# Kernel tuning notes

Measured on AMD Instinct MI355X. Metric: run time of the kernel, lower is better.

Reference implementation:

```python
import jax, jax.numpy as jnp
import numpy as np

B, N, HD = 128, 8192, 256


def setup_inputs() -> dict:
    key = jax.random.key(0)
    ks = jax.random.split(key, 12)
    s = 1.0 / np.sqrt(HD)
    return {
        "encoder_outputs": jax.random.normal(ks[0], (B, N, HD), jnp.float32),
        "hidden": jax.random.normal(ks[1], (B, HD), jnp.float32),
        "cell": jax.random.normal(ks[2], (B, HD), jnp.float32),
        "end_node_embed": jax.random.normal(ks[3], (1, HD), jnp.float32),
        "initial_input": jax.random.normal(ks[4], (B, 3 * HD), jnp.float32),
        # LSTMCell params (PyTorch layout: gates ordered i, f, g, o)
        "W_ih": jax.random.uniform(ks[5], (4 * HD, 3 * HD), jnp.float32, -s, s),
        "b_ih": jax.random.uniform(ks[6], (4 * HD,), jnp.float32, -s, s),
        "W_hh": jax.random.uniform(ks[7], (4 * HD, HD), jnp.float32, -s, s),
        "b_hh": jax.random.uniform(ks[8], (4 * HD,), jnp.float32, -s, s),
        # query_transform Linear params
        "Wq": jax.random.uniform(ks[9], (HD, HD), jnp.float32, -s, s),
        "bq": jax.random.uniform(ks[10], (HD,), jnp.float32, -s, s),
        "max_steps": 10,
    }


def reference(encoder_outputs, hidden, cell, end_node_embed, initial_input,
              W_ih, b_ih, W_hh, b_hh, Wq, bq, max_steps):
    # Prediction mode (teacher_indices=None): feed back top-3 gathered embeddings.
    def step(carry, _):
        h, c, x = carry
        gates = x @ W_ih.T + b_ih + h @ W_hh.T + b_hh        # (B, 4*HD)
        i, f, g, o = jnp.split(gates, 4, axis=-1)
        c_new = jax.nn.sigmoid(f) * c + jax.nn.sigmoid(i) * jnp.tanh(g)
        h_new = jax.nn.sigmoid(o) * jnp.tanh(c_new)
        query = h_new @ Wq.T + bq                            # (B, HD)
        logits = jnp.einsum('bd,bnd->bn', query, encoder_outputs)  # (B, N)
        _, top3 = jax.lax.top_k(logits, 3)                   # (B, 3) int32
        vecs = jnp.take_along_axis(encoder_outputs, top3[..., None], axis=1)  # (B, 3, HD)
        x_next = vecs.reshape(x.shape[0], -1)                # (B, 3*HD)
        return (h_new, c_new, x_next), (logits, top3)
    _, (logits_all, idx_all) = jax.lax.scan(
        step, (hidden, cell, initial_input), None, length=max_steps)
    return logits_all, idx_all  # (max_steps, B, N), (max_steps, B, 3)
```

## Files before the change

### kernel.cpp

```cpp
#include <hip/hip_runtime.h>

typedef unsigned short u16;
typedef unsigned int   u32;

#define B_    128
#define N_    8192
#define HD_   256
#define X_    768
#define T_    10
#define SEGS_ 16
#define SEGROWS_ 512

__device__ float g_h[B_*HD_];
__device__ float g_c[B_*HD_];
__device__ float g_q[B_*HD_];
__device__ float g_pval[B_*SEGS_*3];
__device__ int   g_pidx[B_*SEGS_*3];
__device__ int   g_isf32;

__device__ __forceinline__ float bf2f(u16 u){ return __uint_as_float(((u32)u)<<16); }
__device__ __forceinline__ float lo2f(u32 w){ return __uint_as_float(w<<16); }
__device__ __forceinline__ float hi2f(u32 w){ return __uint_as_float(w & 0xffff0000u); }
__device__ __forceinline__ u16 f2bf(float f){
  u32 u = __float_as_uint(f);
  u32 r = u + 0x7fffu + ((u>>16)&1u);
  return (u16)(r>>16);
}

template<bool F32>
__device__ __forceinline__ float ld1(const void* p, size_t i){
  if constexpr (F32) return ((const float*)p)[i];
  else               return bf2f(((const u16*)p)[i]);
}

template<bool F32>
__device__ __forceinline__ void st1(void* p, size_t i, float v){
  if constexpr (F32) ((float*)p)[i] = v;
  else               ((u16*)p)[i]   = f2bf(v);
}

template<bool F32>
__device__ __forceinline__ void ld8(const void* p, size_t i, float* o){
  if constexpr (F32){
    const float4* q = (const float4*)((const float*)p + i);
    float4 a = q[0], b = q[1];
    o[0]=a.x; o[1]=a.y; o[2]=a.z; o[3]=a.w;
    o[4]=b.x; o[5]=b.y; o[6]=b.z; o[7]=b.w;
  } else {
    uint4 u = *(const uint4*)((const u16*)p + i);
    o[0]=lo2f(u.x); o[1]=hi2f(u.x); o[2]=lo2f(u.y); o[3]=hi2f(u.y);
    o[4]=lo2f(u.z); o[5]=hi2f(u.z); o[6]=lo2f(u.w); o[7]=hi2f(u.w);
  }
}

__device__ __forceinline__ void t3ins(float v,int i,
    float&v0,int&i0,float&v1,int&i1,float&v2,int&i2){
  if (v>v0 || (v==v0 && i<i0)) { v2=v1;i2=i1; v1=v0;i1=i0; v0=v;i0=i; }
  else if (v>v1 || (v==v1 && i<i1)) { v2=v1;i2=i1; v1=v;i1=i; }
  else if (v>v2 || (v==v2 && i<i2)) { v2=v;i2=i; }
}

__global__ void k_probe(const void* enc){
  const int lane = threadIdx.x;
  const u16 u = ((const u16*)enc)[lane*2];
  const float a = fabsf(bf2f(u));
  const bool inr = (a >= 0.0009765625f) && (a <= 1024.0f);
  unsigned long long m = __ballot(inr ? 1 : 0);
  if (lane==0) g_isf32 = (__popcll(m) < 32) ? 1 : 0;
}

template<bool F32>
__device__ void lstm_body(const void* enc, const void* h0, const void* c0,
  const void* x0, const void* Wih, const void* bih, const void* Whh,
  const void* bhh, const void* Wq, const void* bq, void* out, int t)
{
  const int b = blockIdx.x, d = threadIdx.x;
  __shared__ float xs[X_];
  __shared__ float hs[HD_];
  __shared__ float hn[HD_];
  __shared__ int   idx3[3];

  float cd;
  if (t == 0){
    for (int i=d;i<X_;i+=256) xs[i] = ld1<F32>(x0, (size_t)b*X_+i);
    hs[d] = ld1<F32>(h0, (size_t)b*HD_+d);
    cd    = ld1<F32>(c0, (size_t)b*HD_+d);
  } else {
    if (d==0){
      float v0=-3.4e38f,v1=-3.4e38f,v2=-3.4e38f; int i0=-1,i1=-1,i2=-1;
      const float* pv = g_pval + b*SEGS_*3;
      const int*   pi = g_pidx + b*SEGS_*3;
      for (int s=0;s<SEGS_*3;s++) t3ins(pv[s],pi[s],v0,i0,v1,i1,v2,i2);
      idx3[0]=i0; idx3[1]=i1; idx3[2]=i2;
      const size_t ib = (size_t)T_*B_*N_ + (size_t)(t-1)*B_*3 + (size_t)b*3;
      st1<F32>(out, ib+0, (float)i0);
      st1<F32>(out, ib+1, (float)i1);
      st1<F32>(out, ib+2, (float)i2);
    }
    __syncthreads();
    #pragma unroll
    for (int j=0;j<3;j++){
      int jj = idx3[j]; jj = jj<0 ? 0 : (jj>N_-1 ? N_-1 : jj);
      xs[j*HD_+d] = ld1<F32>(enc, ((size_t)b*N_ + jj)*HD_ + d);
    }
    hs[d] = g_h[b*HD_+d];
    cd    = g_c[b*HD_+d];
  }
  __syncthreads();

  float g4[4];
  #pragma unroll
  for (int gi=0;gi<4;gi++){
    const int row = gi*HD_ + d;
    float acc = ld1<F32>(bih,row) + ld1<F32>(bhh,row);
    #pragma unroll 4
    for (int kk=0;kk<X_/8;kk++){
      float w[8]; ld8<F32>(Wih, (size_t)row*X_ + kk*8, w);
      #pragma unroll
      for (int j=0;j<8;j++) acc = fmaf(xs[kk*8+j], w[j], acc);
    }
    #pragma unroll 4
    for (int kk=0;kk<HD_/8;kk++){
      float w[8]; ld8<F32>(Whh, (size_t)row*HD_ + kk*8, w);
      #pragma unroll
      for (int j=0;j<8;j++) acc = fmaf(hs[kk*8+j], w[j], acc);
    }
    g4[gi]=acc;
  }
  const float sig_i = 1.f/(1.f+expf(-g4[0]));
  const float sig_f = 1.f/(1.f+expf(-g4[1]));
  const float tan_g = tanhf(g4[2]);
  const float sig_o = 1.f/(1.f+expf(-g4[3]));
  const float cn = sig_f*cd + sig_i*tan_g;
  const float hv = sig_o*tanhf(cn);
  g_c[b*HD_+d]=cn; g_h[b*HD_+d]=hv; hn[d]=hv;
  __syncthreads();

  float acc = ld1<F32>(bq,d);
  #pragma unroll 4
  for (int kk=0;kk<HD_/8;kk++){
    float w[8]; ld8<F32>(Wq, (size_t)d*HD_ + kk*8, w);
    #pragma unroll
    for (int j=0;j<8;j++) acc = fmaf(hn[kk*8+j], w[j], acc);
  }
  g_q[b*HD_+d]=acc;
}

__global__ __launch_bounds__(256) void k_lstm(
  const void* enc, const void* h0, const void* c0, const void* x0,
  const void* Wih, const void* bih, const void* Whh, const void* bhh,
  const void* Wq, const void* bq, void* out, int t)
{
  if (g_isf32) lstm_body<true >(enc,h0,c0,x0,Wih,bih,Whh,bhh,Wq,bq,out,t);
  else         lstm_body<false>(enc,h0,c0,x0,Wih,bih,Whh,bhh,Wq,bq,out,t);
}

template<bool F32>
__device__ void logits_body(const void* enc, void* out, int t)
{
  const int seg = blockIdx.x, b = blockIdx.y;
  const int tid  = threadIdx.x;
  const int wave = tid>>6;
  const int lane = tid&63;
  const int kl   = lane&31;
  const int half = lane>>5;

  float qv[8];
  const float* qb = g_q + b*HD_ + kl*8;
  #pragma unroll
  for (int j=0;j<8;j++) qv[j]=qb[j];

  float v0=-3.4e38f,v1=-3.4e38f,v2=-3.4e38f; int i0=-1,i1=-1,i2=-1;
  const size_t rowbase = (size_t)b*N_ + seg*SEGROWS_;
  const size_t obase   = (size_t)t*B_*N_ + rowbase;

  #pragma unroll 2
  for (int it=0; it<SEGROWS_/8; ++it){
    const int n = (it*4 + wave)*2 + half;
    float w[8]; ld8<F32>(enc, (rowbase + n)*HD_ + kl*8, w);
    float acc =       qv[0]*w[0];
    acc = fmaf(qv[1], w[1], acc);
    acc = fmaf(qv[2], w[2], acc);
    acc = fmaf(qv[3], w[3], acc);
    acc = fmaf(qv[4], w[4], acc);
    acc = fmaf(qv[5], w[5], acc);
    acc = fmaf(qv[6], w[6], acc);
    acc = fmaf(qv[7], w[7], acc);
    #pragma unroll
    for (int off=16; off>=1; off>>=1)
      acc += __shfl_xor(acc, off, 64);
    if (kl==0) st1<F32>(out, obase + n, acc);
    t3ins(acc, seg*SEGROWS_+n, v0,i0,v1,i1,v2,i2);
  }

  __shared__ float sv[8][3];
  __shared__ int   si[8][3];
  if (kl==0){
    const int slot = wave*2+half;
    sv[slot][0]=v0; sv[slot][1]=v1; sv[slot][2]=v2;
    si[slot][0]=i0; si[slot][1]=i1; si[slot][2]=i2;
  }
  __syncthreads();
  if (tid==0){
    float w0=-3.4e38f,w1=-3.4e38f,w2=-3.4e38f; int j0=-1,j1=-1,j2=-1;
    for (int s=0;s<8;s++)
      for (int k=0;k<3;k++)
        t3ins(sv[s][k],si[s][k],w0,j0,w1,j1,w2,j2);
    float* pv = g_pval + (b*SEGS_+seg)*3;
    int*   pi = g_pidx + (b*SEGS_+seg)*3;
    pv[0]=w0; pv[1]=w1; pv[2]=w2;
    pi[0]=j0; pi[1]=j1; pi[2]=j2;
  }
}

__global__ __launch_bounds__(256) void k_logits(const void* enc, void* out, int t)
{
  if (g_isf32) logits_body<true >(enc,out,t);
  else         logits_body<false>(enc,out,t);
}

__global__ void k_final(void* out)
{
  const int b = blockIdx.x;
  if (threadIdx.x==0){
    float v0=-3.4e38f,v1=-3.4e38f,v2=-3.4e38f; int i0=-1,i1=-1,i2=-1;
    const float* pv = g_pval + b*SEGS_*3;
    const int*   pi = g_pidx + b*SEGS_*3;
    for (int s=0;s<SEGS_*3;s++) t3ins(pv[s],pi[s],v0,i0,v1,i1,v2,i2);
    const size_t ib = (size_t)T_*B_*N_ + (size_t)(T_-1)*B_*3 + (size_t)b*3;
    if (g_isf32){
      ((float*)out)[ib+0]=(float)i0;
      ((float*)out)[ib+1]=(float)i1;
      ((float*)out)[ib+2]=(float)i2;
    } else {
      ((u16*)out)[ib+0]=f2bf((float)i0);
      ((u16*)out)[ib+1]=f2bf((float)i1);
      ((u16*)out)[ib+2]=f2bf((float)i2);
    }
  }
}

extern "C" void kernel_launch(void* const* d_in, const int* in_sizes, int n_in,
                              void* d_out, int out_size, void* d_ws, size_t ws_size,
                              hipStream_t stream)
{
  (void)in_sizes; (void)n_in; (void)out_size; (void)d_ws; (void)ws_size;
  const void* enc = d_in[0];
  const void* h0  = d_in[1];
  const void* c0  = d_in[2];
  const void* x0  = d_in[4];
  const void* Wih = d_in[5];
  const void* bih = d_in[6];
  const void* Whh = d_in[7];
  const void* bhh = d_in[8];
  const void* Wq  = d_in[9];
  const void* bq  = d_in[10];

  k_probe<<<dim3(1),dim3(64),0,stream>>>(enc);

  for (int t=0;t<T_;t++){
    k_lstm<<<dim3(B_),dim3(256),0,stream>>>(enc,h0,c0,x0,Wih,bih,Whh,bhh,Wq,bq,
                                            d_out, t);
    k_logits<<<dim3(SEGS_,B_),dim3(256),0,stream>>>(enc, d_out, t);
  }
  k_final<<<dim3(B_),dim3(64),0,stream>>>(d_out);
}
```

Before: 4.655 ms.

## Fuse all timesteps into one persistent cooperative kernel with grid syncs

Replaces the 21 per-step kernel launches with a single cooperative persistent kernel. Blocks loop over the LSTM and logits work for each timestep and separate the phases with grid.sync(). The logits work is also regrouped into fewer, larger segments: 8 segments of 1024 rows instead of 16 of 512. This is meant to remove launch and drain gaps between the small LSTM kernel and the large logits kernel. In exchange it adds grid-wide barrier cost, and the LSTM phase only uses 128 blocks, leaving the rest idle at each step. If the cooperative launch is unavailable, the code falls back to the multi-kernel path.

```diff
diff --git a/kernel.cpp b/kernel.cpp
--- a/kernel.cpp
+++ b/kernel.cpp
@@ -1,4 +1,7 @@
 #include <hip/hip_runtime.h>
+#include <hip/hip_cooperative_groups.h>
+
+namespace cg = cooperative_groups;
 
 typedef unsigned short u16;
 typedef unsigned int   u32;
@@ -8,8 +11,9 @@
 #define HD_   256
 #define X_    768
 #define T_    10
-#define SEGS_ 16
-#define SEGROWS_ 512
+#define SEGS_ 8
+#define SEGROWS_ 1024
+#define PAIRS_ (B_*SEGS_)
 
 __device__ float g_h[B_*HD_];
 __device__ float g_c[B_*HD_];
@@ -17,6 +21,11 @@
 __device__ float g_pval[B_*SEGS_*3];
 __device__ int   g_pidx[B_*SEGS_*3];
 __device__ int   g_isf32;
+
+struct P {
+  const void *enc, *h0, *c0, *x0, *Wih, *bih, *Whh, *bhh, *Wq, *bq;
+  void* out;
+};
 
 __device__ __forceinline__ float bf2f(u16 u){ return __uint_as_float(((u32)u)<<16); }
 __device__ __forceinline__ float lo2f(u32 w){ return __uint_as_float(w<<16); }
@@ -70,11 +79,9 @@
 }
 
 template<bool F32>
-__device__ void lstm_body(const void* enc, const void* h0, const void* c0,
-  const void* x0, const void* Wih, const void* bih, const void* Whh,
-  const void* bhh, const void* Wq, const void* bq, void* out, int t)
-{
-  const int b = blockIdx.x, d = threadIdx.x;
+__device__ void lstm_b(const P& p, int t, int b)
+{
+  const int d = threadIdx.x;
   __shared__ float xs[X_];
   __shared__ float hs[HD_];
   __shared__ float hn[HD_];
@@ -82,9 +89,9 @@
 
   float cd;
   if (t == 0){
-    for (int i=d;i<X_;i+=256) xs[i] = ld1<F32>(x0, (size_t)b*X_+i);
-    hs[d] = ld1<F32>(h0, (size_t)b*HD_+d);
-    cd    = ld1<F32>(c0, (size_t)b*HD_+d);
+    for (int i=d;i<X_;i+=256) xs[i] = ld1<F32>(p.x0, (size_t)b*X_+i);
+    hs[d] = ld1<F32>(p.h0, (size_t)b*HD_+d);
+    cd    = ld1<F32>(p.c0, (size_t)b*HD_+d);
   } else {
     if (d==0){
       float v0=-3.4e38f,v1=-3.4e38f,v2=-3.4e38f; int i0=-1,i1=-1,i2=-1;
@@ -93,15 +100,15 @@
       for (int s=0;s<SEGS_*3;s++) t3ins(pv[s],pi[s],v0,i0,v1,i1,v2,i2);
       idx3[0]=i0; idx3[1]=i1; idx3[2]=i2;
       const size_t ib = (size_t)T_*B_*N_ + (size_t)(t-1)*B_*3 + (size_t)b*3;
-      st1<F32>(out, ib+0, (float)i0);
-      st1<F32>(out, ib+1, (float)i1);
-      st1<F32>(out, ib+2, (float)i2);
+      st1<F32>(p.out, ib+0, (float)i0);
+      st1<F32>(p.out, ib+1, (float)i1);
+      st1<F32>(p.out, ib+2, (float)i2);
     }
     __syncthreads();
     #pragma unroll
     for (int j=0;j<3;j++){
       int jj = idx3[j]; jj = jj<0 ? 0 : (jj>N_-1 ? N_-1 : jj);
-      xs[j*HD_+d] = ld1<F32>(enc, ((size_t)b*N_ + jj)*HD_ + d);
+      xs[j*HD_+d] = ld1<F32>(p.enc, ((size_t)b*N_ + jj)*HD_ + d);
     }
     hs[d] = g_h[b*HD_+d];
     cd    = g_c[b*HD_+d];
@@ -112,16 +119,16 @@
   #pragma unroll
   for (int gi=0;gi<4;gi++){
     const int row = gi*HD_ + d;
-    float acc = ld1<F32>(bih,row) + ld1<F32>(bhh,row);
+    float acc = ld1<F32>(p.bih,row) + ld1<F32>(p.bhh,row);
     #pragma unroll 4
     for (int kk=0;kk<X_/8;kk++){
-      float w[8]; ld8<F32>(Wih, (size_t)row*X_ + kk*8, w);
+      float w[8]; ld8<F32>(p.Wih, (size_t)row*X_ + kk*8, w);
       #pragma unroll
       for (int j=0;j<8;j++) acc = fmaf(xs[kk*8+j], w[j], acc);
     }
     #pragma unroll 4
     for (int kk=0;kk<HD_/8;kk++){
-      float w[8]; ld8<F32>(Whh, (size_t)row*HD_ + kk*8, w);
+      float w[8]; ld8<F32>(p.Whh, (size_t)row*HD_ + kk*8, w);
       #pragma unroll
       for (int j=0;j<8;j++) acc = fmaf(hs[kk*8+j], w[j], acc);
     }
@@ -136,29 +143,19 @@
   g_c[b*HD_+d]=cn; g_h[b*HD_+d]=hv; hn[d]=hv;
   __syncthreads();
 
-  float acc = ld1<F32>(bq,d);
+  float acc = ld1<F32>(p.bq,d);
   #pragma unroll 4
   for (int kk=0;kk<HD_/8;kk++){
-    float w[8]; ld8<F32>(Wq, (size_t)d*HD_ + kk*8, w);
+    float w[8]; ld8<F32>(p.Wq, (size_t)d*HD_ + kk*8, w);
     #pragma unroll
     for (int j=0;j<8;j++) acc = fmaf(hn[kk*8+j], w[j], acc);
   }
   g_q[b*HD_+d]=acc;
 }
 
-__global__ __launch_bounds__(256) void k_lstm(
-  const void* enc, const void* h0, const void* c0, const void* x0,
-  const void* Wih, const void* bih, const void* Whh, const void* bhh,
-  const void* Wq, const void* bq, void* out, int t)
-{
-  if (g_isf32) lstm_body<true >(enc,h0,c0,x0,Wih,bih,Whh,bhh,Wq,bq,out,t);
-  else         lstm_body<false>(enc,h0,c0,x0,Wih,bih,Whh,bhh,Wq,bq,out,t);
-}
-
-template<bool F32>
-__device__ void logits_body(const void* enc, void* out, int t)
-{
-  const int seg = blockIdx.x, b = blockIdx.y;
+template<bool F32>
+__device__ void logits_b(const P& p, int t, int b, int seg)
+{
   const int tid  = threadIdx.x;
   const int wave = tid>>6;
   const int lane = tid&63;
@@ -171,13 +168,13 @@
   for (int j=0;j<8;j++) qv[j]=qb[j];
 
   float v0=-3.4e38f,v1=-3.4e38f,v2=-3.4e38f; int i0=-1,i1=-1,i2=-1;
-  const size_t rowbase = (size_t)b*N_ + seg*SEGROWS_;
+  const size_t rowbase = (size_t)b*N_ + (size_t)seg*SEGROWS_;
   const size_t obase   = (size_t)t*B_*N_ + rowbase;
 
   #pragma unroll 2
   for (int it=0; it<SEGROWS_/8; ++it){
     const int n = (it*4 + wave)*2 + half;
-    float w[8]; ld8<F32>(enc, (rowbase + n)*HD_ + kl*8, w);
+    float w[8]; ld8<F32>(p.enc, (rowbase + n)*HD_ + kl*8, w);
     float acc =       qv[0]*w[0];
     acc = fmaf(qv[1], w[1], acc);
     acc = fmaf(qv[2], w[2], acc);
@@ -189,7 +186,7 @@
     #pragma unroll
     for (int off=16; off>=1; off>>=1)
       acc += __shfl_xor(acc, off, 64);
-    if (kl==0) st1<F32>(out, obase + n, acc);
+    if (kl==0) st1<F32>(p.out, obase + n, acc);
     t3ins(acc, seg*SEGROWS_+n, v0,i0,v1,i1,v2,i2);
   }
 
@@ -211,33 +208,62 @@
     pv[0]=w0; pv[1]=w1; pv[2]=w2;
     pi[0]=j0; pi[1]=j1; pi[2]=j2;
   }
-}
-
-__global__ __launch_bounds__(256) void k_logits(const void* enc, void* out, int t)
-{
-  if (g_isf32) logits_body<true >(enc,out,t);
-  else         logits_body<false>(enc,out,t);
-}
-
-__global__ void k_final(void* out)
-{
-  const int b = blockIdx.x;
+  __syncthreads();
+}
+
+template<bool F32>
+__device__ void final_b(const P& p, int b)
+{
   if (threadIdx.x==0){
     float v0=-3.4e38f,v1=-3.4e38f,v2=-3.4e38f; int i0=-1,i1=-1,i2=-1;
     const float* pv = g_pval + b*SEGS_*3;
     const int*   pi = g_pidx + b*SEGS_*3;
     for (int s=0;s<SEGS_*3;s++) t3ins(pv[s],pi[s],v0,i0,v1,i1,v2,i2);
     const size_t ib = (size_t)T_*B_*N_ + (size_t)(T_-1)*B_*3 + (size_t)b*3;
-    if (g_isf32){
-      ((float*)out)[ib+0]=(float)i0;
-      ((float*)out)[ib+1]=(float)i1;
-      ((float*)out)[ib+2]=(float)i2;
-    } else {
-      ((u16*)out)[ib+0]=f2bf((float)i0);
-      ((u16*)out)[ib+1]=f2bf((float)i1);
-      ((u16*)out)[ib+2]=f2bf((float)i2);
-    }
-  }
+    st1<F32>(p.out, ib+0, (float)i0);
+    st1<F32>(p.out, ib+1, (float)i1);
+    st1<F32>(p.out, ib+2, (float)i2);
+  }
+}
+
+template<bool F32>
+__device__ void run_all(const P& p)
+{
+  cg::grid_group grid = cg::this_grid();
+  for (int t=0;t<T_;t++){
+    for (int b=blockIdx.x; b<B_; b+=gridDim.x)
+      lstm_b<F32>(p, t, b);
+    grid.sync();
+    for (int pr=blockIdx.x; pr<PAIRS_; pr+=gridDim.x)
+      logits_b<F32>(p, t, pr>>3, pr&7);
+    grid.sync();
+  }
+  for (int b=blockIdx.x; b<B_; b+=gridDim.x)
+    final_b<F32>(p, b);
+}
+
+__global__ __launch_bounds__(256) void k_all(P p)
+{
+  if (g_isf32) run_all<true >(p);
+  else         run_all<false>(p);
+}
+
+__global__ __launch_bounds__(256) void k_lstm(P p, int t)
+{
+  if (g_isf32) lstm_b<true >(p, t, blockIdx.x);
+  else         lstm_b<false>(p, t, blockIdx.x);
+}
+
+__global__ __launch_bounds__(256) void k_logits(P p, int t)
+{
+  if (g_isf32) logits_b<true >(p, t, blockIdx.y, blockIdx.x);
+  else         logits_b<false>(p, t, blockIdx.y, blockIdx.x);
+}
+
+__global__ void k_final(P p)
+{
+  if (g_isf32) final_b<true >(p, blockIdx.x);
+  else         final_b<false>(p, blockIdx.x);
 }
 
 extern "C" void kernel_launch(void* const* d_in, const int* in_sizes, int n_in,
@@ -245,23 +271,40 @@
                               hipStream_t stream)
 {
   (void)in_sizes; (void)n_in; (void)out_size; (void)d_ws; (void)ws_size;
-  const void* enc = d_in[0];
-  const void* h0  = d_in[1];
-  const void* c0  = d_in[2];
-  const void* x0  = d_in[4];
-  const void* Wih = d_in[5];
-  const void* bih = d_in[6];
-  const void* Whh = d_in[7];
-  const void* bhh = d_in[8];
-  const void* Wq  = d_in[9];
-  const void* bq  = d_in[10];
-
-  k_probe<<<dim3(1),dim3(64),0,stream>>>(enc);
-
-  for (int t=0;t<T_;t++){
-    k_lstm<<<dim3(B_),dim3(256),0,stream>>>(enc,h0,c0,x0,Wih,bih,Whh,bhh,Wq,bq,
-                                            d_out, t);
-    k_logits<<<dim3(SEGS_,B_),dim3(256),0,stream>>>(enc, d_out, t);
-  }
-  k_final<<<dim3(B_),dim3(64),0,stream>>>(d_out);
-}
+  P p;
+  p.enc = d_in[0];
+  p.h0  = d_in[1];
+  p.c0  = d_in[2];
+  p.x0  = d_in[4];
+  p.Wih = d_in[5];
+  p.bih = d_in[6];
+  p.Whh = d_in[7];
+  p.bhh = d_in[8];
+  p.Wq  = d_in[9];
+  p.bq  = d_in[10];
+  p.out = d_out;
+
+  k_probe<<<dim3(1),dim3(64),0,stream>>>(p.enc);
+
+  int occ = 0;
+  hipError_t oe = hipOccupancyMaxActiveBlocksPerMultiprocessor(&occ, k_all, 256, 0);
+  bool done = false;
+  if (oe == hipSuccess && occ > 0){
+    int nb = occ * 256;
+    if (nb > PAIRS_) nb = PAIRS_;
+    if (nb >= 128){
+      void* args[] = { (void*)&p };
+      hipError_t le = hipLaunchCooperativeKernel((void*)k_all, dim3(nb), dim3(256),
+                                                 args, 0, stream);
+      done = (le == hipSuccess);
+    }
+  }
+
+  if (!done){
+    for (int t=0;t<T_;t++){
+      k_lstm  <<<dim3(B_),        dim3(256),0,stream>>>(p, t);
+      k_logits<<<dim3(SEGS_,B_),  dim3(256),0,stream>>>(p, t);
+    }
+    k_final<<<dim3(B_),dim3(64),0,stream>>>(p);
+  }
+}
```

After: 7.898 ms. +69.7%, slower.
